# Kernel optimization log

Measured on AMD Instinct MI355X. Metric: run time of the kernel, lower is better.

Reference implementation:

```python
import jax, jax.numpy as jnp
import numpy as np

DIM = 1024
HEADS = 16
D_K = DIM // HEADS


def setup_inputs() -> dict:
    key = jax.random.key(0)
    k1, k2, k3, k4 = jax.random.split(key, 4)
    s = 1.0 / np.sqrt(DIM)
    return {
        "x": jax.random.normal(k1, (8, 1024, DIM), dtype=jnp.float32),
        "w_qkv": jax.random.uniform(k2, (DIM, 3 * DIM), dtype=jnp.float32, minval=-s, maxval=s),
        "w_out": jax.random.uniform(k3, (DIM, DIM), dtype=jnp.float32, minval=-s, maxval=s),
        "b_out": jax.random.uniform(k4, (DIM,), dtype=jnp.float32, minval=-s, maxval=s),
    }


def reference(x, w_qkv, w_out, b_out):
    B, N, _ = x.shape
    scale = D_K ** -0.5
    qkv = x @ w_qkv                                   # [B, N, 3*dim]
    q, k, v = jnp.split(qkv, 3, axis=-1)
    # [B, N, dim] -> [B, H, N, d_k]
    def heads(t):
        return t.reshape(B, N, HEADS, D_K).transpose(0, 2, 1, 3)
    q, k, v = heads(q), heads(k), heads(v)
    dots = jnp.einsum("bhnd,bhmd->bhnm", q, k) * scale  # [B, H, N, N]
    attn = jax.nn.softmax(dots, axis=-1)
    out = jnp.einsum("bhnm,bhmd->bhnd", attn, v)        # [B, H, N, d_k]
    out = out.transpose(0, 2, 1, 3).reshape(B, N, HEADS * D_K)
    return out @ w_out + b_out
```

## Files before the change

kernel.cpp:

```cpp
#include <hip/hip_runtime.h>
#include <hip/hip_bf16.h>
#include <math.h>


typedef __attribute__((ext_vector_type(8))) _Float16 f16x8;
typedef __attribute__((ext_vector_type(4))) _Float16 f16x4;
typedef __attribute__((ext_vector_type(4))) float f32x4;
typedef __attribute__((ext_vector_type(16))) float f32x16;
typedef __attribute__((ext_vector_type(4))) unsigned int u32x4;

#define QK_SCALE 0.18033688011112042f

#define GLOBAL_LOAD_LDS16(g, l) \
  __builtin_amdgcn_global_load_lds((const __attribute__((address_space(1))) void*)(g), \
                                   (__attribute__((address_space(3))) void*)(l), 16, 0, 0)

__global__ __launch_bounds__(256) void cast_all(
    const float* __restrict__ x, _Float16* __restrict__ xh,
    const float* __restrict__ w_qkv, _Float16* __restrict__ wqT,
    const float* __restrict__ w_out, _Float16* __restrict__ woT) {
  __shared__ _Float16 hs[64][65];
  const int blk = blockIdx.x;
  const int t = threadIdx.x;

  if (blk < 2048) {
    const int n4 = 8192 * 1024 / 4;
    int i = blk * 256 + t;
    const int stride = 2048 * 256;
    for (; i < n4; i += stride) {
      float4 v = ((const float4*)x)[i];
      f16x4 h;
      h[0] = (_Float16)v.x; h[1] = (_Float16)v.y;
      h[2] = (_Float16)v.z; h[3] = (_Float16)v.w;
      ((f16x4*)xh)[i] = h;
    }
    return;
  }

  const float* in;
  _Float16* hi;
  int R, C, bx, by;
  if (blk < 2048 + 768) {
    const int id = blk - 2048;
    in = w_qkv; hi = wqT; R = 1024; C = 3072;
    bx = id % 48; by = id / 48;
  } else {
    const int id = blk - 2816;
    in = w_out; hi = woT; R = 1024; C = 1024;
    bx = id % 16; by = id / 16;
  }
  const int r0 = by * 64, c0 = bx * 64;
#pragma unroll
  for (int it = 0; it < 4; ++it) {
    int r = (t >> 4) + it * 16;
    int cc = (t & 15) * 4;
    float4 v = *(const float4*)(in + (size_t)(r0 + r) * C + c0 + cc);
    hs[r][cc + 0] = (_Float16)v.x;
    hs[r][cc + 1] = (_Float16)v.y;
    hs[r][cc + 2] = (_Float16)v.z;
    hs[r][cc + 3] = (_Float16)v.w;
  }
  __syncthreads();
  const int oc = t >> 2;
  const int rr = (t & 3) * 16;
#pragma unroll
  for (int g = 0; g < 2; ++g) {
    f16x8 a;
#pragma unroll
    for (int j = 0; j < 8; ++j) a[j] = hs[rr + g * 8 + j][oc];
    *(f16x8*)(hi + (size_t)(c0 + oc) * R + r0 + rr + g * 8) = a;
  }
}

__global__ __launch_bounds__(256) void gemm1_qkv(
    const _Float16* __restrict__ Ah, const _Float16* __restrict__ Bh,
    _Float16* __restrict__ qkout, _Float16* __restrict__ vTout) {
  __shared__ char lds[34816];
  const int K = 1024;
  const int tid = threadIdx.x;
  const int wave = tid >> 6, lane = tid & 63;
  const int m0 = blockIdx.y * 128, n0 = blockIdx.x * 128;
  const int wr = wave >> 1, wc = wave & 1;

  const int srow_off = lane >> 3;
  const int slot     = lane & 7;
  const int lr = lane & 15, kg = lane >> 4;

  f32x4 acc[4][4];
#pragma unroll
  for (int m = 0; m < 4; ++m)
#pragma unroll
    for (int n = 0; n < 4; ++n) acc[m][n] = (f32x4){0.f, 0.f, 0.f, 0.f};

  const _Float16* gbase[2];
  gbase[0] = Ah + (size_t)m0 * K;
  gbase[1] = Bh + (size_t)n0 * K;

  for (int k0 = 0; k0 < K; k0 += 64) {
    __syncthreads();
#pragma unroll
    for (int p = 0; p < 2; ++p) {
#pragma unroll
      for (int it = 0; it < 4; ++it) {
        const int rbase = wave * 32 + it * 8;
        const int r  = rbase + srow_off;
        const int gc = slot ^ (r & 7);
        const _Float16* g = gbase[p] + (size_t)r * K + k0 + gc * 8;
        GLOBAL_LOAD_LDS16(g, lds + p * 16384 + rbase * 128);
      }
    }
    __syncthreads();

#pragma unroll
    for (int s2 = 0; s2 < 2; ++s2) {
      f16x8 af[4], bf[4];
      const int c = s2 * 4 + kg;
#pragma unroll
      for (int m = 0; m < 4; ++m) {
        const int e = wr * 64 + m * 16 + lr;
        af[m] = *(const f16x8*)(lds + 0 * 16384 + e * 128 + ((c ^ (e & 7)) * 16));
      }
#pragma unroll
      for (int n = 0; n < 4; ++n) {
        const int e = wc * 64 + n * 16 + lr;
        bf[n] = *(const f16x8*)(lds + 1 * 16384 + e * 128 + ((c ^ (e & 7)) * 16));
      }
#pragma unroll
      for (int m = 0; m < 4; ++m)
#pragma unroll
        for (int n = 0; n < 4; ++n)
          acc[m][n] = __builtin_amdgcn_mfma_f32_16x16x32_f16(af[m], bf[n], acc[m][n], 0, 0, 0);
    }
  }

  const int crow = (lane >> 4) * 4, ccol = lane & 15;
  if (n0 < 2048) {
    const float qsc = (n0 < 1024) ? (float)QK_SCALE : 1.0f;
#pragma unroll
    for (int m = 0; m < 4; ++m) {
#pragma unroll
      for (int n = 0; n < 4; ++n) {
        const int rbase = m0 + wr * 64 + m * 16 + crow;
        const int cc = n0 + wc * 64 + n * 16 + ccol;
#pragma unroll
        for (int i = 0; i < 4; ++i)
          qkout[(size_t)(rbase + i) * 2048 + cc] = (_Float16)(acc[m][n][i] * qsc);
      }
    }
  } else {
    __syncthreads();
    _Float16* lv = (_Float16*)lds;
#pragma unroll
    for (int m = 0; m < 4; ++m)
#pragma unroll
      for (int n = 0; n < 4; ++n) {
        const int cc = wc * 64 + n * 16 + ccol;
#pragma unroll
        for (int i = 0; i < 4; ++i) {
          const int r = wr * 64 + m * 16 + crow + i;
          lv[cc * 136 + r] = (_Float16)acc[m][n][i];
        }
      }
    __syncthreads();
    const int bb = m0 >> 10, seq0 = m0 & 1023;
    const int hbase = (n0 - 2048) >> 6;
#pragma unroll
    for (int it = 0; it < 8; ++it) {
      const int idx = tid + it * 256;
      const int cc = idx >> 4, ch = idx & 15;
      f16x8 v = *(const f16x8*)(lv + cc * 136 + ch * 8);
      const int hh = hbase + (cc >> 6), d = cc & 63;
      *(f16x8*)(vTout + (((size_t)bb * 16 + hh) * 64 + d) * 1024 + seq0 + ch * 8) = v;
    }
  }
}

__global__ __launch_bounds__(256) void attn_mfma(
    const _Float16* __restrict__ qk,
    const _Float16* __restrict__ vT,
    _Float16* __restrict__ ao) {
  const int hb   = blockIdx.x;
  const int h    = hb >> 3;
  const int b    = hb & 7;
  const int band = blockIdx.y;
  const int tid  = threadIdx.x;
  const int wave = tid >> 6;
  const int lane = tid & 63;
  const int l31  = lane & 31;
  const int hi   = lane >> 5;
  const int kswz = (l31 & 7) << 4;

  __shared__ _Float16 Ks[3][64 * 64];
  __shared__ _Float16 Vt[3][64 * 64];

  const _Float16* vbase = vT + ((size_t)(b * 16 + h) * 64) * 1024;

  const int qrow_g = b * 1024 + band * 128 + wave * 32 + l31;
  f16x8 qf[4];
#pragma unroll
  for (int c = 0; c < 4; ++c)
    qf[c] = *(const f16x8*)(qk + (size_t)qrow_g * 2048 + h * 64 + c * 16 + hi * 8);

  f16x8 vones;
#pragma unroll
  for (int j = 0; j < 8; ++j) vones[j] = (_Float16)1.0f;

  f32x16 accO0 = {0}, accO1 = {0}, accL = {0};

  const int srow8 = (lane >> 3);
  const int slot  = lane & 7;

  auto stage_t = [&](int t, int buf) {
#pragma unroll
    for (int it = 0; it < 2; ++it) {
      const int r  = wave * 8 + srow8 + it * 32;
      const int gc = slot ^ (r & 7);
      const _Float16* gk = qk + (size_t)(b * 1024 + t * 64 + r) * 2048 +
                           1024 + h * 64 + gc * 8;
      const _Float16* gv = vbase + (size_t)r * 1024 + t * 64 + gc * 8;
      char* dk = (char*)&Ks[buf][0] + (wave * 8 + it * 32) * 128;
      char* dv = (char*)&Vt[buf][0] + (wave * 8 + it * 32) * 128;
      GLOBAL_LOAD_LDS16(gk, dk);
      GLOBAL_LOAD_LDS16(gv, dv);
    }
  };

  auto compute_tile = [&](const char* ksb, const char* vtb) {
    f32x16 accS0 = {0}, accS1 = {0};
    __builtin_amdgcn_s_setprio(1);
#pragma unroll
    for (int c = 0; c < 4; ++c) {
      f16x8 ka0 = *(const f16x8*)(ksb + l31 * 128 + ((c * 32 + hi * 16) ^ kswz));
      f16x8 ka1 = *(const f16x8*)(ksb + (l31 + 32) * 128 + ((c * 32 + hi * 16) ^ kswz));
      accS0 = __builtin_amdgcn_mfma_f32_32x32x16_f16(ka0, qf[c], accS0, 0, 0, 0);
      accS1 = __builtin_amdgcn_mfma_f32_32x32x16_f16(ka1, qf[c], accS1, 0, 0, 0);
    }
    __builtin_amdgcn_s_setprio(0);

#pragma unroll
    for (int c = 0; c < 4; ++c) {
      float e[8];
#pragma unroll
      for (int k = 0; k < 8; ++k)
        e[k] = __builtin_exp2f((c < 2) ? accS0[(c & 1) * 8 + k]
                                       : accS1[(c & 1) * 8 + k]);
      unsigned q0a = __builtin_bit_cast(unsigned, __builtin_amdgcn_cvt_pkrtz(e[0], e[1]));
      unsigned q0b = __builtin_bit_cast(unsigned, __builtin_amdgcn_cvt_pkrtz(e[2], e[3]));
      unsigned q1a = __builtin_bit_cast(unsigned, __builtin_amdgcn_cvt_pkrtz(e[4], e[5]));
      unsigned q1b = __builtin_bit_cast(unsigned, __builtin_amdgcn_cvt_pkrtz(e[6], e[7]));
      unsigned send_a = hi ? q0a : q1a;
      unsigned send_b = hi ? q0b : q1b;
      unsigned recv_a = __shfl_xor(send_a, 32);
      unsigned recv_b = __shfl_xor(send_b, 32);
      u32x4 pu;
      pu[0] = hi ? recv_a : q0a;
      pu[1] = hi ? recv_b : q0b;
      pu[2] = hi ? q1a : recv_a;
      pu[3] = hi ? q1b : recv_b;
      f16x8 pa = __builtin_bit_cast(f16x8, pu);

      const int kchunk = ((2 * c + hi) * 16) ^ kswz;
      f16x8 vb0 = *(const f16x8*)(vtb + l31 * 128 + kchunk);
      f16x8 vb1 = *(const f16x8*)(vtb + (l31 + 32) * 128 + kchunk);
      __builtin_amdgcn_s_setprio(1);
      accO0 = __builtin_amdgcn_mfma_f32_32x32x16_f16(pa, vb0, accO0, 0, 0, 0);
      accO1 = __builtin_amdgcn_mfma_f32_32x32x16_f16(pa, vb1, accO1, 0, 0, 0);
      accL  = __builtin_amdgcn_mfma_f32_32x32x16_f16(pa, vones, accL, 0, 0, 0);
      __builtin_amdgcn_s_setprio(0);
    }
  };

  stage_t(0, 0);
  stage_t(1, 1);

  for (int t = 0; t < 14; ++t) {
    __builtin_amdgcn_s_barrier();
    stage_t(t + 2, (t + 2) % 3);
    asm volatile("s_waitcnt vmcnt(8)" ::: "memory");
    __builtin_amdgcn_sched_barrier(0);
    __builtin_amdgcn_s_barrier();
    const int bt = t % 3;
    compute_tile((const char*)&Ks[bt][0], (const char*)&Vt[bt][0]);
  }
  asm volatile("s_waitcnt vmcnt(4)" ::: "memory");
  __builtin_amdgcn_sched_barrier(0);
  __builtin_amdgcn_s_barrier();
  compute_tile((const char*)&Ks[2][0], (const char*)&Vt[2][0]);
  asm volatile("s_waitcnt vmcnt(0)" ::: "memory");
  __builtin_amdgcn_sched_barrier(0);
  __builtin_amdgcn_s_barrier();
  compute_tile((const char*)&Ks[0][0], (const char*)&Vt[0][0]);

#pragma unroll
  for (int reg = 0; reg < 16; ++reg) {
    const int qr = (reg & 3) + 8 * (reg >> 2) + 4 * hi;
    const float il = 1.f / accL[reg];
    const size_t grow = (size_t)(b * 1024 + band * 128 + wave * 32 + qr) * 1024 + h * 64;
    ao[grow + l31]      = (_Float16)(accO0[reg] * il);
    ao[grow + 32 + l31] = (_Float16)(accO1[reg] * il);
  }
}

__global__ __launch_bounds__(256) void gemm2_out(
    const _Float16* __restrict__ A,
    const _Float16* __restrict__ B,
    float* __restrict__ C, const float* __restrict__ bias) {
  __shared__ char lds[2 * 16384];
  const int K = 1024;
  const int tid = threadIdx.x;
  const int wave = tid >> 6, lane = tid & 63;
  const int m0 = blockIdx.y * 128, n0 = blockIdx.x * 128;
  const int wr = wave >> 1, wc = wave & 1;

  const int srow_off = lane >> 3;
  const int slot     = lane & 7;
  const int lr = lane & 15, kg = lane >> 4;

  f32x4 acc[4][4];
#pragma unroll
  for (int m = 0; m < 4; ++m)
#pragma unroll
    for (int n = 0; n < 4; ++n) acc[m][n] = (f32x4){0.f, 0.f, 0.f, 0.f};

  const _Float16* gbase[2];
  gbase[0] = A + (size_t)m0 * K;
  gbase[1] = B + (size_t)n0 * K;

  for (int k0 = 0; k0 < K; k0 += 64) {
    __syncthreads();
#pragma unroll
    for (int p = 0; p < 2; ++p) {
#pragma unroll
      for (int it = 0; it < 4; ++it) {
        const int rbase = wave * 32 + it * 8;
        const int r  = rbase + srow_off;
        const int gc = slot ^ (r & 7);
        const _Float16* g = gbase[p] + (size_t)r * K + k0 + gc * 8;
        GLOBAL_LOAD_LDS16(g, lds + p * 16384 + rbase * 128);
      }
    }
    __syncthreads();

#pragma unroll
    for (int s2 = 0; s2 < 2; ++s2) {
      f16x8 af[4], bf[4];
      const int c = s2 * 4 + kg;
#pragma unroll
      for (int m = 0; m < 4; ++m) {
        const int e = wr * 64 + m * 16 + lr;
        af[m] = *(const f16x8*)(lds + 0 * 16384 + e * 128 + ((c ^ (e & 7)) * 16));
      }
#pragma unroll
      for (int n = 0; n < 4; ++n) {
        const int e = wc * 64 + n * 16 + lr;
        bf[n] = *(const f16x8*)(lds + 1 * 16384 + e * 128 + ((c ^ (e & 7)) * 16));
      }
#pragma unroll
      for (int m = 0; m < 4; ++m)
#pragma unroll
        for (int n = 0; n < 4; ++n)
          acc[m][n] = __builtin_amdgcn_mfma_f32_16x16x32_f16(af[m], bf[n], acc[m][n], 0, 0, 0);
    }
  }

  const int crow = (lane >> 4) * 4, ccol = lane & 15;
#pragma unroll
  for (int m = 0; m < 4; ++m) {
#pragma unroll
    for (int n = 0; n < 4; ++n) {
      const int rbase = m0 + wr * 64 + m * 16 + crow;
      const int c = n0 + wc * 64 + n * 16 + ccol;
      const float bv = bias[c];
#pragma unroll
      for (int i = 0; i < 4; ++i)
        C[(size_t)(rbase + i) * 1024 + c] = acc[m][n][i] + bv;
    }
  }
}

extern "C" void kernel_launch(void* const* d_in, const int* in_sizes, int n_in,
                              void* d_out, int out_size, void* d_ws, size_t ws_size,
                              hipStream_t stream) {
  const float* x     = (const float*)d_in[0];
  const float* w_qkv = (const float*)d_in[1];
  const float* w_out = (const float*)d_in[2];
  const float* b_out = (const float*)d_in[3];
  float* out = (float*)d_out;

  char* ws = (char*)d_ws;
  _Float16* xh  = (_Float16*)(ws);
  _Float16* ao  = xh;
  _Float16* wqT = (_Float16*)(ws + (32u << 20));
  _Float16* woT = (_Float16*)(ws + (44u << 20));
  _Float16* qkp = (_Float16*)(ws + (48u << 20));
  _Float16* vT  = (_Float16*)(ws + (80u << 20));

  cast_all<<<3072, 256, 0, stream>>>(x, xh, w_qkv, wqT, w_out, woT);

  gemm1_qkv<<<dim3(24, 64), 256, 0, stream>>>(xh, wqT, qkp, vT);

  attn_mfma<<<dim3(128, 8), 256, 0, stream>>>(qkp, vT, ao);

  gemm2_out<<<dim3(8, 64), 256, 0, stream>>>(ao, woT, out, b_out);
}
```

Before: 175.6 us.

## Double-buffer LDS K-tiles in QKV and output GEMMs with single barrier

Both fp16 MFMA GEMMs now split each 64-wide K step into two 32-wide tiles held in two LDS buffers. The async global-to-LDS load for the next tile is issued before the current tile's MFMAs, so memory latency can overlap compute, and each iteration needs one barrier instead of two. The LDS swizzle is redone for the 64-byte row layout. In exchange there are twice as many loop iterations and barriers, and each iteration does less MFMA work to hide latency behind.

```diff
diff --git a/kernel.cpp b/kernel.cpp
--- a/kernel.cpp
+++ b/kernel.cpp
@@ -82,9 +82,10 @@
   const int m0 = blockIdx.y * 128, n0 = blockIdx.x * 128;
   const int wr = wave >> 1, wc = wave & 1;
 
-  const int srow_off = lane >> 3;
-  const int slot     = lane & 7;
+  const int srow = lane >> 2;
+  const int sgchunk = (lane & 3) ^ ((srow >> 1) & 3);
   const int lr = lane & 15, kg = lane >> 4;
+  const int rdoff = lr * 64 + ((kg ^ ((lr >> 1) & 3)) * 16);
 
   f32x4 acc[4][4];
 #pragma unroll
@@ -96,41 +97,37 @@
   gbase[0] = Ah + (size_t)m0 * K;
   gbase[1] = Bh + (size_t)n0 * K;
 
-  for (int k0 = 0; k0 < K; k0 += 64) {
+  auto stage_g = [&](int t, int buf) {
+#pragma unroll
+    for (int p = 0; p < 2; ++p) {
+#pragma unroll
+      for (int half = 0; half < 2; ++half) {
+        const int r16 = wave * 32 + half * 16;
+        const _Float16* g = gbase[p] + (size_t)(r16 + srow) * K + t * 32 + sgchunk * 8;
+        GLOBAL_LOAD_LDS16(g, lds + (buf * 2 + p) * 8192 + r16 * 64);
+      }
+    }
+  };
+
+  stage_g(0, 0);
+
+  for (int t = 0; t < 32; ++t) {
     __syncthreads();
-#pragma unroll
-    for (int p = 0; p < 2; ++p) {
-#pragma unroll
-      for (int it = 0; it < 4; ++it) {
-        const int rbase = wave * 32 + it * 8;
-        const int r  = rbase + srow_off;
-        const int gc = slot ^ (r & 7);
-        const _Float16* g = gbase[p] + (size_t)r * K + k0 + gc * 8;
-        GLOBAL_LOAD_LDS16(g, lds + p * 16384 + rbase * 128);
-      }
-    }
-    __syncthreads();
-
-#pragma unroll
-    for (int s2 = 0; s2 < 2; ++s2) {
-      f16x8 af[4], bf[4];
-      const int c = s2 * 4 + kg;
-#pragma unroll
-      for (int m = 0; m < 4; ++m) {
-        const int e = wr * 64 + m * 16 + lr;
-        af[m] = *(const f16x8*)(lds + 0 * 16384 + e * 128 + ((c ^ (e & 7)) * 16));
-      }
-#pragma unroll
-      for (int n = 0; n < 4; ++n) {
-        const int e = wc * 64 + n * 16 + lr;
-        bf[n] = *(const f16x8*)(lds + 1 * 16384 + e * 128 + ((c ^ (e & 7)) * 16));
-      }
-#pragma unroll
-      for (int m = 0; m < 4; ++m)
-#pragma unroll
-        for (int n = 0; n < 4; ++n)
-          acc[m][n] = __builtin_amdgcn_mfma_f32_16x16x32_f16(af[m], bf[n], acc[m][n], 0, 0, 0);
-    }
+    if (t < 31) stage_g(t + 1, (t + 1) & 1);
+    const char* base = lds + (t & 1) * 16384;
+
+    f16x8 af[4], bf[4];
+#pragma unroll
+    for (int m = 0; m < 4; ++m)
+      af[m] = *(const f16x8*)(base + 0 * 8192 + (wr * 64 + m * 16) * 64 + rdoff);
+#pragma unroll
+    for (int n = 0; n < 4; ++n)
+      bf[n] = *(const f16x8*)(base + 1 * 8192 + (wc * 64 + n * 16) * 64 + rdoff);
+#pragma unroll
+    for (int m = 0; m < 4; ++m)
+#pragma unroll
+      for (int n = 0; n < 4; ++n)
+        acc[m][n] = __builtin_amdgcn_mfma_f32_16x16x32_f16(af[m], bf[n], acc[m][n], 0, 0, 0);
   }
 
   const int crow = (lane >> 4) * 4, ccol = lane & 15;
@@ -312,9 +309,10 @@
   const int m0 = blockIdx.y * 128, n0 = blockIdx.x * 128;
   const int wr = wave >> 1, wc = wave & 1;
 
-  const int srow_off = lane >> 3;
-  const int slot     = lane & 7;
+  const int srow = lane >> 2;
+  const int sgchunk = (lane & 3) ^ ((srow >> 1) & 3);
   const int lr = lane & 15, kg = lane >> 4;
+  const int rdoff = lr * 64 + ((kg ^ ((lr >> 1) & 3)) * 16);
 
   f32x4 acc[4][4];
 #pragma unroll
@@ -326,41 +324,37 @@
   gbase[0] = A + (size_t)m0 * K;
   gbase[1] = B + (size_t)n0 * K;
 
-  for (int k0 = 0; k0 < K; k0 += 64) {
+  auto stage_g = [&](int t, int buf) {
+#pragma unroll
+    for (int p = 0; p < 2; ++p) {
+#pragma unroll
+      for (int half = 0; half < 2; ++half) {
+        const int r16 = wave * 32 + half * 16;
+        const _Float16* g = gbase[p] + (size_t)(r16 + srow) * K + t * 32 + sgchunk * 8;
+        GLOBAL_LOAD_LDS16(g, lds + (buf * 2 + p) * 8192 + r16 * 64);
+      }
+    }
+  };
+
+  stage_g(0, 0);
+
+  for (int t = 0; t < 32; ++t) {
     __syncthreads();
-#pragma unroll
-    for (int p = 0; p < 2; ++p) {
-#pragma unroll
-      for (int it = 0; it < 4; ++it) {
-        const int rbase = wave * 32 + it * 8;
-        const int r  = rbase + srow_off;
-        const int gc = slot ^ (r & 7);
-        const _Float16* g = gbase[p] + (size_t)r * K + k0 + gc * 8;
-        GLOBAL_LOAD_LDS16(g, lds + p * 16384 + rbase * 128);
-      }
-    }
-    __syncthreads();
-
-#pragma unroll
-    for (int s2 = 0; s2 < 2; ++s2) {
-      f16x8 af[4], bf[4];
-      const int c = s2 * 4 + kg;
-#pragma unroll
-      for (int m = 0; m < 4; ++m) {
-        const int e = wr * 64 + m * 16 + lr;
-        af[m] = *(const f16x8*)(lds + 0 * 16384 + e * 128 + ((c ^ (e & 7)) * 16));
-      }
-#pragma unroll
-      for (int n = 0; n < 4; ++n) {
-        const int e = wc * 64 + n * 16 + lr;
-        bf[n] = *(const f16x8*)(lds + 1 * 16384 + e * 128 + ((c ^ (e & 7)) * 16));
-      }
-#pragma unroll
-      for (int m = 0; m < 4; ++m)
-#pragma unroll
-        for (int n = 0; n < 4; ++n)
-          acc[m][n] = __builtin_amdgcn_mfma_f32_16x16x32_f16(af[m], bf[n], acc[m][n], 0, 0, 0);
-    }
+    if (t < 31) stage_g(t + 1, (t + 1) & 1);
+    const char* base = lds + (t & 1) * 16384;
+
+    f16x8 af[4], bf[4];
+#pragma unroll
+    for (int m = 0; m < 4; ++m)
+      af[m] = *(const f16x8*)(base + 0 * 8192 + (wr * 64 + m * 16) * 64 + rdoff);
+#pragma unroll
+    for (int n = 0; n < 4; ++n)
+      bf[n] = *(const f16x8*)(base + 1 * 8192 + (wc * 64 + n * 16) * 64 + rdoff);
+#pragma unroll
+    for (int m = 0; m < 4; ++m)
+#pragma unroll
+      for (int n = 0; n < 4; ++n)
+        acc[m][n] = __builtin_amdgcn_mfma_f32_16x16x32_f16(af[m], bf[n], acc[m][n], 0, 0, 0);
   }
 
   const int crow = (lane >> 4) * 4, ccol = lane & 15;
```

New measurement: 184.1 us. 1.05x slower.
